# Kernel tuning notes

Measured on AMD Instinct MI355X. Metric: run time of the kernel, lower is better.

The kernel has to match this reference:

```python
import jax, jax.numpy as jnp
import numpy as np

N_CLASSES = 64
K_NEIGHBORS = 10
ITERATIONS = 3
IN_DIM = 512
D_MODEL = 256
N_SUPPORT = 2048
N_QUERY = 6144


def setup_inputs() -> dict:
    key = jax.random.key(0)
    k1, k2, k3, k4 = jax.random.split(key, 4)
    support = jax.random.normal(k1, (1, N_SUPPORT, IN_DIM), dtype=jnp.float32)
    query = jax.random.normal(k2, (1, N_QUERY, IN_DIM), dtype=jnp.float32)
    support_labels = jax.random.randint(k3, (N_SUPPORT,), 0, N_CLASSES)
    W = jax.random.normal(k4, (IN_DIM, D_MODEL), dtype=jnp.float32) / np.sqrt(IN_DIM)
    return {"support": support, "query": query, "support_labels": support_labels, "W": W}


def reference(support, query, support_labels, W):
    n_way = N_CLASSES
    ns = support.shape[1]
    nq = query.shape[1]

    # encoder: linear projection
    s_emb = jnp.einsum('bnd,de->bne', support, W)   # (1, ns, D)
    q_emb = jnp.einsum('bnd,de->bne', query, W)     # (1, nq, D)
    all_emb = jnp.concatenate([s_emb, q_emb], axis=1)  # (1, n, D)

    # prototypes (computed in the original forward; unused downstream)
    onehot_s = jax.nn.one_hot(support_labels, n_way, dtype=s_emb.dtype)  # (ns, C)
    counts = onehot_s.sum(0)
    protos = (onehot_s.T @ s_emb[0]) / jnp.maximum(counts, 1.0)[:, None]

    # kNN graph via cdist + topk(smallest) + scatter
    x = all_emb[0]                                  # (n, D)
    n = x.shape[0]
    sq = jnp.sum(x * x, axis=-1)
    d2 = sq[:, None] + sq[None, :] - 2.0 * (x @ x.T)
    dist = jnp.sqrt(jnp.maximum(d2, 0.0))           # (n, n)
    k = min(K_NEIGHBORS, n - 1)
    _, idx = jax.lax.top_k(-dist, k)                # k nearest (incl. self)
    adj = jnp.zeros((n, n), dtype=jnp.float32)
    adj = adj.at[jnp.arange(n)[:, None], idx].set(1.0)
    adj = ((adj + adj.T) > 0).astype(jnp.float32)   # symmetrize

    # row-normalized transition and label propagation
    deg = adj.sum(axis=1, keepdims=True)
    deg = jnp.where(deg == 0, 1.0, deg)
    trans = adj / deg
    label_mat = jnp.concatenate(
        [onehot_s, jnp.zeros((nq, n_way), dtype=jnp.float32)], axis=0)  # (n, C)
    labels = label_mat
    for _ in range(ITERATIONS):
        labels = trans @ labels

    pred = jnp.argmax(labels, axis=-1)              # (n,)
    query_pred = pred[ns:]
    logits = jax.nn.one_hot(query_pred, n_way, dtype=jnp.float32)[None]  # (1, nq, C)
    # protos participates in the original forward; keep it live (no-op add of zeros)
    logits = logits + 0.0 * jnp.sum(protos) * 0.0
    return logits
```

## Files before the change

kernel.cpp:

```cpp
#include <hip/hip_runtime.h>
#include <stdint.h>

#define NS   2048
#define NQ   6144
#define NN   8192
#define IND  512
#define DM   256
#define KNB  10
#define NSPLIT 8
#define PCAP 1536

#define AS1 __attribute__((address_space(1)))
#define AS3 __attribute__((address_space(3)))

typedef short bf16x8 __attribute__((ext_vector_type(8)));
typedef float f32x4  __attribute__((ext_vector_type(4)));
typedef unsigned long long u64;

__device__ __forceinline__ unsigned short f2bf(float v)
{
    unsigned int u = __float_as_uint(v);
    unsigned int r = (u + 0x7fffu + ((u >> 16) & 1u)) >> 16;
    return (unsigned short)r;
}
__device__ __forceinline__ float bf2f(unsigned short h)
{
    return __uint_as_float(((unsigned int)h) << 16);
}

__device__ __forceinline__ void key_insert(u64 key, u64 K[KNB])
{
    u64 cur = key;
#pragma unroll
    for (int s = 0; s < KNB; ++s) {
        u64 lo = (cur < K[s]) ? cur : K[s];
        u64 hi = (cur < K[s]) ? K[s] : cur;
        K[s] = lo; cur = hi;
    }
}

__global__ __launch_bounds__(256) void wpack_kernel(const float* __restrict__ W,
                                                    bf16x8* __restrict__ Wthi,
                                                    bf16x8* __restrict__ Wtlo)
{
    int f = blockIdx.x * 256 + threadIdx.x;
    int dim = f & 255, qp = (f >> 8) & 3, c = f >> 10;
    int k0 = 32 * c + 8 * qp;
    bf16x8 h8, l8;
#pragma unroll
    for (int j = 0; j < 8; ++j) {
        float v = W[(size_t)(k0 + j) * DM + dim];
        unsigned short hu = f2bf(v);
        float hf = bf2f(hu);
        unsigned short lu = f2bf(v - hf);
        h8[j] = (short)hu; l8[j] = (short)lu;
    }
    Wthi[f] = h8; Wtlo[f] = l8;
}

__global__ __launch_bounds__(256) void embed_kernel(
    const float* __restrict__ support, const float* __restrict__ query,
    const bf16x8* __restrict__ Wthi, const bf16x8* __restrict__ Wtlo,
    bf16x8* __restrict__ Ghi, bf16x8* __restrict__ Glo, float* __restrict__ sq)
{
    __shared__ __align__(16) char lds[36928];
    bf16x8* Ehf = reinterpret_cast<bf16x8*>(lds);
    bf16x8* Elf = Ehf + 1024;
    float*  et  = reinterpret_cast<float*>(lds);
    float*  sqred = reinterpret_cast<float*>(lds + 32768);
    const int t = threadIdx.x;
    const int l = t & 63, w = t >> 6;
    const int lm = l & 15, q = l >> 4;
    const int i0 = blockIdx.x * 16;

    {
        const int node = t & 15;
        const int g = i0 + node;
        const float* src = (g < NS) ? (support + (size_t)g * IND)
                                    : (query + (size_t)(g - NS) * IND);
#pragma unroll
        for (int i = 0; i < 4; ++i) {
            int cq = (t >> 4) + 16 * i;
            const float* p = src + cq * 8;
            float4 v0 = *reinterpret_cast<const float4*>(p);
            float4 v1 = *reinterpret_cast<const float4*>(p + 4);
            float vv[8] = {v0.x, v0.y, v0.z, v0.w, v1.x, v1.y, v1.z, v1.w};
            bf16x8 h8, l8;
#pragma unroll
            for (int j = 0; j < 8; ++j) {
                unsigned short hu = f2bf(vv[j]);
                float hf = bf2f(hu);
                unsigned short lu = f2bf(vv[j] - hf);
                h8[j] = (short)hu; l8[j] = (short)lu;
            }
            Ehf[cq * 16 + node] = h8;
            Elf[cq * 16 + node] = l8;
        }
    }
    __syncthreads();

    f32x4 acc[4];
#pragma unroll
    for (int nt = 0; nt < 4; ++nt) acc[nt] = (f32x4){0.f, 0.f, 0.f, 0.f};
    const int dimb = 64 * w + lm;
    for (int c = 0; c < 16; ++c) {
        const bf16x8 Anh = Ehf[(c * 4 + q) * 16 + lm];
        const bf16x8 Anl = Elf[(c * 4 + q) * 16 + lm];
        const int fb = c * 1024 + q * 256 + dimb;
#pragma unroll
        for (int nt = 0; nt < 4; ++nt) {
            const bf16x8 Wh = Wthi[fb + 16 * nt];
            const bf16x8 Wl = Wtlo[fb + 16 * nt];
            f32x4 a = acc[nt];
            a = __builtin_amdgcn_mfma_f32_16x16x32_bf16(Anh, Wh, a, 0, 0, 0);
            a = __builtin_amdgcn_mfma_f32_16x16x32_bf16(Anh, Wl, a, 0, 0, 0);
            a = __builtin_amdgcn_mfma_f32_16x16x32_bf16(Anl, Wh, a, 0, 0, 0);
            a = __builtin_amdgcn_mfma_f32_16x16x32_bf16(Anl, Wl, a, 0, 0, 0);
            acc[nt] = a;
        }
    }
    __syncthreads();

#pragma unroll
    for (int r = 0; r < 4; ++r) {
        float s = 0.f;
#pragma unroll
        for (int nt = 0; nt < 4; ++nt) {
            float v = acc[nt][r];
            et[(4 * q + r) * 260 + dimb + 16 * nt] = v;
            s += v * v;
        }
        sqred[(4 * q + r) * 65 + w * 16 + lm] = s;
    }
    __syncthreads();

#pragma unroll
    for (int i = 0; i < 2; ++i) {
        int f = t + 256 * i;
        int node = f & 15, qd = (f >> 4) & 3, cd = f >> 6;
        const float* ep = &et[node * 260 + 32 * cd + 8 * qd];
        bf16x8 h8, l8;
#pragma unroll
        for (int j = 0; j < 8; ++j) {
            float v = ep[j];
            unsigned short hu = f2bf(v);
            float hf = bf2f(hu);
            unsigned short lu = f2bf(v - hf);
            h8[j] = (short)hu; l8[j] = (short)lu;
        }
        size_t gi = (size_t)(cd * 4 + qd) * NN + i0 + node;
        Ghi[gi] = h8;
        Glo[gi] = l8;
    }
    if (t < 16) {
        float s = 0.f;
#pragma unroll
        for (int x = 0; x < 64; ++x) s += sqred[t * 65 + x];
        sq[i0 + t] = s;
    }
}

__global__ __launch_bounds__(256, 2) void dist_topk_kernel(
    const bf16x8* __restrict__ Ghi, const bf16x8* __restrict__ Glo,
    const float* __restrict__ sq, u64* __restrict__ cand)
{
    __shared__ bf16x8 stage[2][1024];
    __shared__ u64 stk[4][256];
    const int t  = threadIdx.x;
    const int l  = t & 63, w = t >> 6;
    const int lm = l & 15, q = l >> 4;
    const int i0 = blockIdx.x * 64;
    const int row = i0 + 16 * w + lm;
    const int split = blockIdx.y;

    const float  sqi    = sq[row];
    const size_t rowIdx = (size_t)q * NN + row;

    u64 K[KNB];
#pragma unroll
    for (int s = 0; s < KNB; ++s) K[s] = ~0ull;
    u64 thr = ~0ull;
    u64 thr_row = ~0ull;
    int cnt = 0;

    auto drain = [&]() {
        u64 live = __ballot(cnt > 0);
        while (live) {
            if (cnt > 0) {
                --cnt;
                u64 key = stk[cnt][t];
                if (key < thr) {
                    key_insert(key, K);
                    thr = K[KNB - 1];
                }
            }
            live = __ballot(cnt > 0);
        }
    };

    auto stage_issue = [&](int it, int b) {
        const int jt = split * 8 + (it >> 3);
        const int c  = it & 7;
        const int j0 = jt * 128;
        const size_t cbase = (size_t)c * (NN * 4);
        const bool hi = (w < 2);
        const int  wf = (w & 1) * 256;
        const bf16x8* gsel = hi ? Ghi : Glo;
#pragma unroll
        for (int u = 0; u < 4; ++u) {
            const int f  = wf + u * 64;
            const int qr = f >> 7, col0 = f & 127;
            const bf16x8* g = gsel + cbase + (size_t)qr * NN + j0 + col0 + l;
            __builtin_amdgcn_global_load_lds((const AS1 void*)g,
                                             (AS3 void*)&stage[b][(hi ? 0 : 512) + f],
                                             16, 0, 0);
        }
    };

    stage_issue(0, 0);
    __syncthreads();

    f32x4 acc[8];
    for (int it = 0; it < 64; ++it) {
        const int c = it & 7;
        const int b = it & 1;
        if (it + 1 < 64) stage_issue(it + 1, (it + 1) & 1);
        if (c == 0) {
#pragma unroll
            for (int mt = 0; mt < 8; ++mt) acc[mt] = (f32x4){0.f, 0.f, 0.f, 0.f};
        }
        const size_t co = (size_t)c * (NN * 4);
        const bf16x8 Bh = Ghi[co + rowIdx];
        const bf16x8 Bl = Glo[co + rowIdx];
        const bf16x8* sh = &stage[b][0];
        const bf16x8* sl = &stage[b][512];
        const int fq = q * 128 + lm;
#pragma unroll
        for (int mt = 0; mt < 8; ++mt) {
            const int fi = fq + 16 * mt;
            const bf16x8 Ah = sh[fi];
            const bf16x8 Al = sl[fi];
            f32x4 a = acc[mt];
            a = __builtin_amdgcn_mfma_f32_16x16x32_bf16(Ah, Bh, a, 0, 0, 0);
            a = __builtin_amdgcn_mfma_f32_16x16x32_bf16(Ah, Bl, a, 0, 0, 0);
            a = __builtin_amdgcn_mfma_f32_16x16x32_bf16(Al, Bh, a, 0, 0, 0);
            acc[mt] = a;
        }
        if (c == 7) {
            const int j0 = split * 1024 + (it >> 3) * 128;
#pragma unroll
            for (int mt = 0; mt < 8; ++mt) {
                const int jb = j0 + 16 * mt + 4 * q;
                const f32x4 sqj = *reinterpret_cast<const f32x4*>(&sq[jb]);
#pragma unroll
                for (int r = 0; r < 4; ++r) {
                    float d2 = fmaxf(sqi + sqj[r] - 2.0f * acc[mt][r], 0.0f);
                    u64 key = ((u64)__float_as_uint(d2) << 32) | (unsigned)(jb + r);
                    if (key < thr_row) { stk[cnt][t] = key; ++cnt; }
                }
                drain();
            }
            u64 tr = K[KNB - 1];
            u64 o  = __shfl_xor(tr, 16, 64); tr = (o < tr) ? o : tr;
            o      = __shfl_xor(tr, 32, 64); tr = (o < tr) ? o : tr;
            thr_row = tr;
        }
        __syncthreads();
    }
    __syncthreads();
    u64* dump = reinterpret_cast<u64*>(&stage[0][0]);
#pragma unroll
    for (int s = 0; s < KNB; ++s) dump[t * KNB + s] = K[s];
    if (q == 0) {
#pragma unroll
        for (int qq = 1; qq < 4; ++qq)
#pragma unroll
            for (int s = 0; s < KNB; ++s) {
                u64 key = dump[(t + qq * 16) * KNB + s];
                if (key < thr) {
                    key_insert(key, K);
                    thr = K[KNB - 1];
                }
            }
        size_t base = (size_t)row * (NSPLIT * KNB) + split * KNB;
#pragma unroll
        for (int s = 0; s < KNB; ++s) cand[base + s] = K[s];
    }
}

__global__ __launch_bounds__(64) void merge_adj_kernel(
    const u64* __restrict__ cand, unsigned int* __restrict__ bits)
{
    int i = blockIdx.x * 64 + threadIdx.x;
    if (i >= NN) return;
    const u64* cp = cand + (size_t)i * (NSPLIT * KNB);
    u64 K[KNB];
#pragma unroll
    for (int s = 0; s < KNB; ++s) K[s] = cp[s];
    u64 thr = K[KNB - 1];
    for (int s = KNB; s < NSPLIT * KNB; s += KNB) {
        u64 kk[KNB];
#pragma unroll
        for (int e = 0; e < KNB; ++e) kk[e] = cp[s + e];
#pragma unroll
        for (int e = 0; e < KNB; ++e) {
            if (kk[e] < thr) { key_insert(kk[e], K); thr = K[KNB - 1]; }
        }
    }
#pragma unroll
    for (int s = 0; s < KNB; ++s) {
        int j = (int)(K[s] & 0xFFFFFFFFu);
        atomicOr(&bits[(size_t)i * 256 + (j >> 5)], 1u << (j & 31));
        atomicOr(&bits[(size_t)j * 256 + (i >> 5)], 1u << (i & 31));
    }
}

__device__ __forceinline__ int build_list(const unsigned int* __restrict__ row,
                                          int c, int* __restrict__ lst)
{
    unsigned int mw[4];
#pragma unroll
    for (int k = 0; k < 4; ++k) mw[k] = row[4 * c + k];
    int cnt = __popc(mw[0]) + __popc(mw[1]) + __popc(mw[2]) + __popc(mw[3]);
    int incl = cnt;
#pragma unroll
    for (int d = 1; d < 64; d <<= 1) {
        int nb = __shfl_up(incl, d, 64);
        if (c >= d) incl += nb;
    }
    const int off = incl - cnt;
    const int deg = __shfl(incl, 63, 64);
    if (deg <= PCAP) {
        int p = off;
#pragma unroll
        for (int k = 0; k < 4; ++k) {
            unsigned int m = mw[k];
            while (m) {
                int b = __ffs(m) - 1;
                m &= m - 1;
                lst[p++] = (4 * c + k) * 32 + b;
            }
        }
    }
    return deg;
}

__device__ __forceinline__ float prop_gather(const unsigned int* __restrict__ row,
                                             int c, int* __restrict__ lst,
                                             const float* __restrict__ lin)
{
    const int deg = build_list(row, c, lst);
    const float tinv = 1.0f / (float)deg;
    float acc = 0.f;
    if (deg <= PCAP) {
        int d = 0;
        for (; d + 8 <= deg; d += 8) {
            float x[8];
#pragma unroll
            for (int e = 0; e < 8; ++e) x[e] = lin[(size_t)lst[d + e] * 64 + c];
#pragma unroll
            for (int e = 0; e < 8; ++e) acc += __fmul_rn(tinv, x[e]);
        }
        if (d + 4 <= deg) {
            float x[4];
#pragma unroll
            for (int e = 0; e < 4; ++e) x[e] = lin[(size_t)lst[d + e] * 64 + c];
#pragma unroll
            for (int e = 0; e < 4; ++e) acc += __fmul_rn(tinv, x[e]);
            d += 4;
        }
        for (; d < deg; ++d) {
            int j = lst[d];
            acc += __fmul_rn(tinv, lin[(size_t)j * 64 + c]);
        }
    } else {
        for (int w2 = 0; w2 < 256; ++w2) {
            unsigned int m = row[w2];
            while (m) {
                int b = __ffs(m) - 1; m &= m - 1;
                int j = w2 * 32 + b;
                acc += __fmul_rn(tinv, lin[(size_t)j * 64 + c]);
            }
        }
    }
    return acc;
}

__device__ __forceinline__ float prop_init_body(const unsigned int* __restrict__ row,
                                                int c, int* __restrict__ lst,
                                                const int* __restrict__ slab)
{
    const int deg = build_list(row, c, lst);
    const float tinv = 1.0f / (float)deg;
    float acc = 0.f;
    if (deg <= PCAP) {
        for (int d = 0; d < deg; ++d) {
            int j = lst[d];
            float v = (j < NS && slab[j] == c) ? 1.0f : 0.0f;
            acc += __fmul_rn(tinv, v);
        }
    } else {
        for (int w2 = 0; w2 < 256; ++w2) {
            unsigned int m = row[w2];
            while (m) {
                int b = __ffs(m) - 1; m &= m - 1;
                int j = w2 * 32 + b;
                float v = (j < NS && slab[j] == c) ? 1.0f : 0.0f;
                acc += __fmul_rn(tinv, v);
            }
        }
    }
    return acc;
}

__global__ __launch_bounds__(256) void prop_init_kernel(
    const unsigned int* __restrict__ bits, const int* __restrict__ slab,
    float* __restrict__ lout)
{
    __shared__ int lists[4][PCAP];
    const int grp = threadIdx.x >> 6;
    const int c   = threadIdx.x & 63;
    const int i   = blockIdx.x * 4 + grp;
    const unsigned int* row = bits + (size_t)i * 256;
    lout[(size_t)i * 64 + c] = prop_init_body(row, c, lists[grp], slab);
}

__global__ __launch_bounds__(256) void prop_kernel(
    const unsigned int* __restrict__ bits, const float* __restrict__ lin,
    float* __restrict__ lout)
{
    __shared__ int lists[4][PCAP];
    const int grp = threadIdx.x >> 6;
    const int c   = threadIdx.x & 63;
    const int i   = blockIdx.x * 4 + grp;
    const unsigned int* row = bits + (size_t)i * 256;
    lout[(size_t)i * 64 + c] = prop_gather(row, c, lists[grp], lin);
}

__global__ __launch_bounds__(256) void prop_argmax_kernel(
    const unsigned int* __restrict__ bits, const float* __restrict__ lin,
    float* __restrict__ out)
{
    __shared__ int lists[4][PCAP];
    const int grp = threadIdx.x >> 6;
    const int c   = threadIdx.x & 63;
    const int qn  = blockIdx.x * 4 + grp;
    const int i   = NS + qn;
    const unsigned int* row = bits + (size_t)i * 256;
    float acc = prop_gather(row, c, lists[grp], lin);
    float bv = acc; int bi = c;
#pragma unroll
    for (int off = 32; off >= 1; off >>= 1) {
        float ov = __shfl_xor(bv, off, 64);
        int   oi = __shfl_xor(bi, off, 64);
        if (ov > bv || (ov == bv && oi < bi)) { bv = ov; bi = oi; }
    }
    out[(size_t)qn * 64 + c] = (c == bi) ? 1.0f : 0.0f;
}

extern "C" void kernel_launch(void* const* d_in, const int* in_sizes, int n_in,
                              void* d_out, int out_size, void* d_ws, size_t ws_size,
                              hipStream_t stream)
{
    const float* support = (const float*)d_in[0];
    const float* query   = (const float*)d_in[1];
    const int*   slab    = (const int*)d_in[2];
    const float* W       = (const float*)d_in[3];
    float* out = (float*)d_out;
    char*  ws  = (char*)d_ws;

    const size_t GHI_OFF = 0;
    const size_t GLO_OFF = 4194304;
    const size_t SQ_OFF  = 8388608;
    const size_t CV_OFF  = 8421376;
    const size_t CI_OFF  = CV_OFF + (size_t)NN * NSPLIT * KNB * 4;

    bf16x8*       Ghi  = (bf16x8*)(ws + GHI_OFF);
    bf16x8*       Glo  = (bf16x8*)(ws + GLO_OFF);
    unsigned int* bits = (unsigned int*)(ws + GHI_OFF);
    float*        sq   = (float*)(ws + SQ_OFF);
    bf16x8*       Wthi = (bf16x8*)(ws + CV_OFF);
    bf16x8*       Wtlo = (bf16x8*)(ws + CV_OFF + 262144);
    u64*          cand = (u64*)  (ws + CV_OFF);
    float*        la   = (float*)(ws + CV_OFF);
    float*        lb   = (float*)(ws + CI_OFF);

    wpack_kernel<<<64, 256, 0, stream>>>(W, Wthi, Wtlo);
    embed_kernel<<<512, 256, 0, stream>>>(support, query, Wthi, Wtlo, Ghi, Glo, sq);
    dist_topk_kernel<<<dim3(128, NSPLIT), 256, 0, stream>>>(Ghi, Glo, sq, cand);
    hipMemsetAsync(bits, 0, (size_t)NN * 256 * sizeof(unsigned int), stream);
    merge_adj_kernel<<<NN / 64, 64, 0, stream>>>(cand, bits);
    prop_init_kernel<<<NN / 4, 256, 0, stream>>>(bits, slab, lb);
    prop_kernel<<<NN / 4, 256, 0, stream>>>(bits, lb, la);
    prop_argmax_kernel<<<NQ / 4, 256, 0, stream>>>(bits, la, out);
}
```

Measured before the change: 418.5 us.

## Cache compact CSR neighbor lists from init pass for later propagation steps

The first propagation kernel now writes each row's degree and, when degree is at most 32, a fixed-stride CSR list of neighbor indices. The two later propagation kernels read this list directly instead of rescanning the 8192-bit adjacency row with a wave-wide prefix scan each time. Rows with higher degree fall back to a per-thread serial bit walk over the full row, which is slower than the old LDS list path for those rows. Workspace regions are reassigned, with degA aliasing the squared-norm buffer and csr placed after the label buffers.

```diff
diff --git a/kernel.cpp b/kernel.cpp
--- a/kernel.cpp
+++ b/kernel.cpp
@@ -9,6 +9,7 @@
 #define KNB  10
 #define NSPLIT 8
 #define PCAP 1536
+#define CSTR 32
 
 #define AS1 __attribute__((address_space(1)))
 #define AS3 __attribute__((address_space(3)))
@@ -345,55 +346,94 @@
     return deg;
 }
 
-__device__ __forceinline__ float prop_gather(const unsigned int* __restrict__ row,
-                                             int c, int* __restrict__ lst,
+__device__ __forceinline__ float walk_gather(const unsigned int* __restrict__ row,
+                                             int c, float tinv,
                                              const float* __restrict__ lin)
 {
-    const int deg = build_list(row, c, lst);
+    float acc = 0.f;
+    for (int w2 = 0; w2 < 256; ++w2) {
+        unsigned int m = row[w2];
+        while (m) {
+            int b = __ffs(m) - 1; m &= m - 1;
+            int j = w2 * 32 + b;
+            acc += __fmul_rn(tinv, lin[(size_t)j * 64 + c]);
+        }
+    }
+    return acc;
+}
+
+__device__ __forceinline__ float list_gather(const int* __restrict__ lst, int deg,
+                                             int c, float tinv,
+                                             const float* __restrict__ lin)
+{
+    float acc = 0.f;
+    int d = 0;
+    for (; d + 8 <= deg; d += 8) {
+        float x[8];
+#pragma unroll
+        for (int e = 0; e < 8; ++e) x[e] = lin[(size_t)lst[d + e] * 64 + c];
+#pragma unroll
+        for (int e = 0; e < 8; ++e) acc += __fmul_rn(tinv, x[e]);
+    }
+    if (d + 4 <= deg) {
+        float x[4];
+#pragma unroll
+        for (int e = 0; e < 4; ++e) x[e] = lin[(size_t)lst[d + e] * 64 + c];
+#pragma unroll
+        for (int e = 0; e < 4; ++e) acc += __fmul_rn(tinv, x[e]);
+        d += 4;
+    }
+    for (; d < deg; ++d)
+        acc += __fmul_rn(tinv, lin[(size_t)lst[d] * 64 + c]);
+    return acc;
+}
+
+__device__ __forceinline__ float csr_gather(const int* __restrict__ crow, int deg,
+                                            int c, float tinv,
+                                            const float* __restrict__ lin)
+{
+    float acc = 0.f;
+    int d = 0;
+    for (; d + 8 <= deg; d += 8) {
+        int jj[8];
+#pragma unroll
+        for (int e = 0; e < 8; ++e) jj[e] = crow[d + e];
+        float x[8];
+#pragma unroll
+        for (int e = 0; e < 8; ++e) x[e] = lin[(size_t)jj[e] * 64 + c];
+#pragma unroll
+        for (int e = 0; e < 8; ++e) acc += __fmul_rn(tinv, x[e]);
+    }
+    if (d + 4 <= deg) {
+        int jj[4];
+#pragma unroll
+        for (int e = 0; e < 4; ++e) jj[e] = crow[d + e];
+        float x[4];
+#pragma unroll
+        for (int e = 0; e < 4; ++e) x[e] = lin[(size_t)jj[e] * 64 + c];
+#pragma unroll
+        for (int e = 0; e < 4; ++e) acc += __fmul_rn(tinv, x[e]);
+        d += 4;
+    }
+    for (; d < deg; ++d)
+        acc += __fmul_rn(tinv, lin[(size_t)crow[d] * 64 + c]);
+    return acc;
+}
+
+__global__ __launch_bounds__(256) void prop_init_kernel(
+    const unsigned int* __restrict__ bits, const int* __restrict__ slab,
+    float* __restrict__ lout, int* __restrict__ csr, int* __restrict__ degA)
+{
+    __shared__ int lists[4][PCAP];
+    const int grp = threadIdx.x >> 6;
+    const int c   = threadIdx.x & 63;
+    const int i   = blockIdx.x * 4 + grp;
+    const unsigned int* row = bits + (size_t)i * 256;
+    const int deg = build_list(row, c, lists[grp]);
     const float tinv = 1.0f / (float)deg;
     float acc = 0.f;
     if (deg <= PCAP) {
-        int d = 0;
-        for (; d + 8 <= deg; d += 8) {
-            float x[8];
-#pragma unroll
-            for (int e = 0; e < 8; ++e) x[e] = lin[(size_t)lst[d + e] * 64 + c];
-#pragma unroll
-            for (int e = 0; e < 8; ++e) acc += __fmul_rn(tinv, x[e]);
-        }
-        if (d + 4 <= deg) {
-            float x[4];
-#pragma unroll
-            for (int e = 0; e < 4; ++e) x[e] = lin[(size_t)lst[d + e] * 64 + c];
-#pragma unroll
-            for (int e = 0; e < 4; ++e) acc += __fmul_rn(tinv, x[e]);
-            d += 4;
-        }
-        for (; d < deg; ++d) {
-            int j = lst[d];
-            acc += __fmul_rn(tinv, lin[(size_t)j * 64 + c]);
-        }
-    } else {
-        for (int w2 = 0; w2 < 256; ++w2) {
-            unsigned int m = row[w2];
-            while (m) {
-                int b = __ffs(m) - 1; m &= m - 1;
-                int j = w2 * 32 + b;
-                acc += __fmul_rn(tinv, lin[(size_t)j * 64 + c]);
-            }
-        }
-    }
-    return acc;
-}
-
-__device__ __forceinline__ float prop_init_body(const unsigned int* __restrict__ row,
-                                                int c, int* __restrict__ lst,
-                                                const int* __restrict__ slab)
-{
-    const int deg = build_list(row, c, lst);
-    const float tinv = 1.0f / (float)deg;
-    float acc = 0.f;
-    if (deg <= PCAP) {
+        const int* lst = lists[grp];
         for (int d = 0; d < deg; ++d) {
             int j = lst[d];
             float v = (j < NS && slab[j] == c) ? 1.0f : 0.0f;
@@ -410,44 +450,42 @@
             }
         }
     }
-    return acc;
-}
-
-__global__ __launch_bounds__(256) void prop_init_kernel(
-    const unsigned int* __restrict__ bits, const int* __restrict__ slab,
+    lout[(size_t)i * 64 + c] = acc;
+    if (c == 0) degA[i] = deg;
+    if (deg <= CSTR && c < CSTR)
+        csr[(size_t)i * CSTR + c] = (c < deg) ? lists[grp][c] : 0;
+}
+
+__global__ __launch_bounds__(256) void prop_kernel(
+    const unsigned int* __restrict__ bits, const int* __restrict__ csr,
+    const int* __restrict__ degA, const float* __restrict__ lin,
     float* __restrict__ lout)
 {
-    __shared__ int lists[4][PCAP];
     const int grp = threadIdx.x >> 6;
     const int c   = threadIdx.x & 63;
     const int i   = blockIdx.x * 4 + grp;
-    const unsigned int* row = bits + (size_t)i * 256;
-    lout[(size_t)i * 64 + c] = prop_init_body(row, c, lists[grp], slab);
-}
-
-__global__ __launch_bounds__(256) void prop_kernel(
-    const unsigned int* __restrict__ bits, const float* __restrict__ lin,
-    float* __restrict__ lout)
-{
-    __shared__ int lists[4][PCAP];
-    const int grp = threadIdx.x >> 6;
-    const int c   = threadIdx.x & 63;
-    const int i   = blockIdx.x * 4 + grp;
-    const unsigned int* row = bits + (size_t)i * 256;
-    lout[(size_t)i * 64 + c] = prop_gather(row, c, lists[grp], lin);
+    const int deg = degA[i];
+    const float tinv = 1.0f / (float)deg;
+    float acc;
+    if (deg <= CSTR) acc = csr_gather(csr + (size_t)i * CSTR, deg, c, tinv, lin);
+    else             acc = walk_gather(bits + (size_t)i * 256, c, tinv, lin);
+    lout[(size_t)i * 64 + c] = acc;
 }
 
 __global__ __launch_bounds__(256) void prop_argmax_kernel(
-    const unsigned int* __restrict__ bits, const float* __restrict__ lin,
+    const unsigned int* __restrict__ bits, const int* __restrict__ csr,
+    const int* __restrict__ degA, const float* __restrict__ lin,
     float* __restrict__ out)
 {
-    __shared__ int lists[4][PCAP];
     const int grp = threadIdx.x >> 6;
     const int c   = threadIdx.x & 63;
     const int qn  = blockIdx.x * 4 + grp;
     const int i   = NS + qn;
-    const unsigned int* row = bits + (size_t)i * 256;
-    float acc = prop_gather(row, c, lists[grp], lin);
+    const int deg = degA[i];
+    const float tinv = 1.0f / (float)deg;
+    float acc;
+    if (deg <= CSTR) acc = csr_gather(csr + (size_t)i * CSTR, deg, c, tinv, lin);
+    else             acc = walk_gather(bits + (size_t)i * 256, c, tinv, lin);
     float bv = acc; int bi = c;
 #pragma unroll
     for (int off = 32; off >= 1; off >>= 1) {
@@ -473,24 +511,25 @@
     const size_t GLO_OFF = 4194304;
     const size_t SQ_OFF  = 8388608;
     const size_t CV_OFF  = 8421376;
-    const size_t CI_OFF  = CV_OFF + (size_t)NN * NSPLIT * KNB * 4;
 
     bf16x8*       Ghi  = (bf16x8*)(ws + GHI_OFF);
     bf16x8*       Glo  = (bf16x8*)(ws + GLO_OFF);
     unsigned int* bits = (unsigned int*)(ws + GHI_OFF);
     float*        sq   = (float*)(ws + SQ_OFF);
+    int*          degA = (int*)  (ws + SQ_OFF);
     bf16x8*       Wthi = (bf16x8*)(ws + CV_OFF);
     bf16x8*       Wtlo = (bf16x8*)(ws + CV_OFF + 262144);
     u64*          cand = (u64*)  (ws + CV_OFF);
-    float*        la   = (float*)(ws + CV_OFF);
-    float*        lb   = (float*)(ws + CI_OFF);
+    float*        lb   = (float*)(ws + CV_OFF);
+    float*        la   = (float*)(ws + CV_OFF + 2097152);
+    int*          csr  = (int*)  (ws + CV_OFF + 4194304);
 
     wpack_kernel<<<64, 256, 0, stream>>>(W, Wthi, Wtlo);
     embed_kernel<<<512, 256, 0, stream>>>(support, query, Wthi, Wtlo, Ghi, Glo, sq);
     dist_topk_kernel<<<dim3(128, NSPLIT), 256, 0, stream>>>(Ghi, Glo, sq, cand);
     hipMemsetAsync(bits, 0, (size_t)NN * 256 * sizeof(unsigned int), stream);
     merge_adj_kernel<<<NN / 64, 64, 0, stream>>>(cand, bits);
-    prop_init_kernel<<<NN / 4, 256, 0, stream>>>(bits, slab, lb);
-    prop_kernel<<<NN / 4, 256, 0, stream>>>(bits, lb, la);
-    prop_argmax_kernel<<<NQ / 4, 256, 0, stream>>>(bits, la, out);
-}
+    prop_init_kernel<<<NN / 4, 256, 0, stream>>>(bits, slab, lb, csr, degA);
+    prop_kernel<<<NN / 4, 256, 0, stream>>>(bits, csr, degA, lb, la);
+    prop_argmax_kernel<<<NQ / 4, 256, 0, stream>>>(bits, csr, degA, la, out);
+}
```

Result: slower. 618.5 us (+47.8%).
